# Kernel optimization log

Measured on AMD Instinct MI355X. Metric: run time of the kernel, lower is better.

Reference implementation:

```python
import jax, jax.numpy as jnp
import numpy as np

B, S, D = 4, 2048, 1024
H, DK, DV = 16, 64, 64
LN_EPS = 1e-5


def setup_inputs() -> dict:
    key = jax.random.key(0)
    ks = jax.random.split(key, 6)
    x = jax.random.normal(ks[0], (B, S, D), dtype=jnp.float32)
    # causal mask: True = masked position (j > i), broadcast over batch
    causal = jnp.triu(jnp.ones((S, S), dtype=bool), k=1)
    attention_mask = jnp.broadcast_to(causal, (B, S, S))
    scale = 1.0 / np.sqrt(D)
    w_q = jax.random.normal(ks[1], (D, H * DK), dtype=jnp.float32) * scale
    w_k = jax.random.normal(ks[2], (D, H * DK), dtype=jnp.float32) * scale
    w_v = jax.random.normal(ks[3], (D, H * DV), dtype=jnp.float32) * scale
    w_fc = jax.random.normal(ks[4], (H * DV, D), dtype=jnp.float32) * (1.0 / np.sqrt(H * DV))
    ln_gamma = jnp.ones((D,), dtype=jnp.float32)
    ln_beta = jnp.zeros((D,), dtype=jnp.float32)
    return {"x": x, "attention_mask": attention_mask, "w_q": w_q, "w_k": w_k,
            "w_v": w_v, "w_fc": w_fc, "ln_gamma": ln_gamma, "ln_beta": ln_beta}


def _layernorm(y, gamma, beta):
    mu = jnp.mean(y, axis=-1, keepdims=True)
    var = jnp.mean(jnp.square(y - mu), axis=-1, keepdims=True)
    return (y - mu) * jax.lax.rsqrt(var + LN_EPS) * gamma + beta


def reference(x, attention_mask, w_q, w_k, w_v, w_fc, ln_gamma, ln_beta):
    b, s, _ = x.shape
    # projections -> [b, h, s, dk/dv]
    q = (x @ w_q).reshape(b, s, H, DK).transpose(0, 2, 1, 3)
    k = (x @ w_k).reshape(b, s, H, DK).transpose(0, 2, 1, 3)
    v = (x @ w_v).reshape(b, s, H, DV).transpose(0, 2, 1, 3)
    # scaled dot-product attention with mask (True -> -1e9)
    scores = jnp.einsum('bhqd,bhkd->bhqk', q, k) / np.sqrt(DK)
    scores = jnp.where(attention_mask[:, None, :, :], jnp.float32(-1e9), scores)
    attn = jax.nn.softmax(scores, axis=-1)
    context = jnp.einsum('bhqk,bhkd->bhqd', attn, v)
    context = context.transpose(0, 2, 1, 3).reshape(b, s, H * DV)
    output = context @ w_fc
    out = _layernorm(output + x, ln_gamma, ln_beta)
    return out, attn
```

## Files before the change

kernel.cpp:

```cpp
#include <hip/hip_runtime.h>
#include <stdint.h>

#define S_LEN 2048
#define NHEAD 16

typedef short short8 __attribute__((ext_vector_type(8)));
typedef float f32x4 __attribute__((ext_vector_type(4)));
typedef unsigned short u16;

typedef __attribute__((address_space(1))) uint32_t AS1u32;
typedef __attribute__((address_space(3))) uint32_t AS3u32;

#define MFMA16(a, b, c) __builtin_amdgcn_mfma_f32_16x16x32_bf16((a), (b), (c), 0, 0, 0)

__device__ __forceinline__ void gload16(const void* g, void* l) {
  __builtin_amdgcn_global_load_lds((AS1u32*)g, (AS3u32*)l, 16, 0, 0);
}

__device__ __forceinline__ u16 f2bf(float f) {
  union { float f; uint32_t u; } c; c.f = f;
  return (u16)((c.u + 0x7fffu + ((c.u >> 16) & 1u)) >> 16);
}
__device__ __forceinline__ float bf2f(u16 h) {
  union { uint32_t u; float f; } c; c.u = ((uint32_t)h) << 16;
  return c.f;
}

__global__ __launch_bounds__(256) void conv_x_kernel(const float* __restrict__ x,
                                                     u16* __restrict__ xb) {
  size_t i = ((size_t)blockIdx.x * 256 + threadIdx.x) * 4;
  f32x4 v = *(const f32x4*)(x + i);
  union { u16 h[4]; uint2 d; } o;
  o.h[0] = f2bf(v[0]); o.h[1] = f2bf(v[1]); o.h[2] = f2bf(v[2]); o.h[3] = f2bf(v[3]);
  *(uint2*)(xb + i) = o.d;
}

__global__ __launch_bounds__(256) void transpose_w_kernel(
    const float* __restrict__ w0, const float* __restrict__ w1,
    const float* __restrict__ w2, const float* __restrict__ w3,
    u16* __restrict__ o0, u16* __restrict__ o1, u16* __restrict__ o2, u16* __restrict__ o3) {
  int z = blockIdx.z;
  const float* w = (z == 0) ? w0 : (z == 1) ? w1 : (z == 2) ? w2 : w3;
  u16* o = (z == 0) ? o0 : (z == 1) ? o1 : (z == 2) ? o2 : o3;
  float scale = (z == 0) ? 0.125f : 1.0f;
  __shared__ float t[32][33];
  int n0 = blockIdx.x * 32, k0 = blockIdx.y * 32;
  int tx = threadIdx.x & 31, ty = threadIdx.x >> 5;
#pragma unroll
  for (int i = 0; i < 4; ++i) {
    int k = ty * 4 + i;
    t[k][tx] = w[(size_t)(k0 + k) * 1024 + n0 + tx];
  }
  __syncthreads();
#pragma unroll
  for (int i = 0; i < 4; ++i) {
    int n = ty * 4 + i;
    o[(size_t)(n0 + n) * 1024 + k0 + tx] = f2bf(t[tx][n] * scale);
  }
}

__device__ __forceinline__ void gemm_stage(const char* Ab, const char* Bb, u16* As, u16* Bs,
                                           int m0, int n0, int kbyte, int tid) {
#pragma unroll
  for (int i = 0; i < 2; ++i) {
    int cid = i * 256 + tid;
    int row = cid >> 2, c = cid & 3;
    int off = kbyte + ((c ^ ((row >> 1) & 3)) << 4);
    gload16(Ab + (size_t)(m0 + row) * 2048 + off, (char*)As + i * 4096 + (tid & ~63) * 16);
    gload16(Bb + (size_t)(n0 + row) * 2048 + off, (char*)Bs + i * 4096 + (tid & ~63) * 16);
  }
}

__global__ __launch_bounds__(256) void gemm_bt_kernel(
    const u16* __restrict__ A, const u16* __restrict__ BT,
    void* __restrict__ out, int mode) {
  __shared__ u16 As[128 * 32];
  __shared__ u16 Bs[128 * 32];
  const int tid = threadIdx.x;
  const int lane = tid & 63, wv = tid >> 6;
  const int l15 = lane & 15, h16 = lane >> 4;
  const int wr = wv >> 1, wc = wv & 1;
  const int m0 = blockIdx.x * 128, n0 = blockIdx.y * 128;
  const char* Ab = (const char*)A;
  const char* Bb = (const char*)BT;

  f32x4 acc[4][4];
#pragma unroll
  for (int i = 0; i < 4; ++i)
#pragma unroll
    for (int j = 0; j < 4; ++j) acc[i][j] = (f32x4){0.f, 0.f, 0.f, 0.f};

  gemm_stage(Ab, Bb, As, Bs, m0, n0, 0, tid);
  for (int kt = 0; kt < 32; ++kt) {
    __syncthreads();
    short8 a[4], b[4];
#pragma unroll
    for (int mf = 0; mf < 4; ++mf) {
      int row = wr * 64 + mf * 16 + l15;
      a[mf] = *(const short8*)((const char*)As + row * 64 + ((h16 ^ ((row >> 1) & 3)) << 4));
    }
#pragma unroll
    for (int nf = 0; nf < 4; ++nf) {
      int row = wc * 64 + nf * 16 + l15;
      b[nf] = *(const short8*)((const char*)Bs + row * 64 + ((h16 ^ ((row >> 1) & 3)) << 4));
    }
#pragma unroll
    for (int mf = 0; mf < 4; ++mf)
#pragma unroll
      for (int nf = 0; nf < 4; ++nf)
        acc[mf][nf] = MFMA16(a[mf], b[nf], acc[mf][nf]);
    __syncthreads();
    if (kt + 1 < 32) gemm_stage(Ab, Bb, As, Bs, m0, n0, (kt + 1) * 64, tid);
  }

  if (mode == 0) {
    u16* o = (u16*)out;
#pragma unroll
    for (int mf = 0; mf < 4; ++mf)
#pragma unroll
      for (int nf = 0; nf < 4; ++nf)
#pragma unroll
        for (int r = 0; r < 4; ++r) {
          int m = m0 + wr * 64 + mf * 16 + 4 * h16 + r;
          int n = n0 + wc * 64 + nf * 16 + l15;
          int bb = m >> 11, s = m & 2047, hh = n >> 6, dk = n & 63;
          o[(((size_t)(bb * NHEAD + hh) * S_LEN + s) << 6) + dk] = f2bf(acc[mf][nf][r]);
        }
  } else {
    float* o = (float*)out;
#pragma unroll
    for (int mf = 0; mf < 4; ++mf)
#pragma unroll
      for (int nf = 0; nf < 4; ++nf)
#pragma unroll
        for (int r = 0; r < 4; ++r) {
          int m = m0 + wr * 64 + mf * 16 + 4 * h16 + r;
          int n = n0 + wc * 64 + nf * 16 + l15;
          o[(size_t)m * 1024 + n] = acc[mf][nf][r];
        }
  }
}

__global__ __launch_bounds__(256) void transpose_v_kernel(
    const u16* __restrict__ v, u16* __restrict__ vT) {
  __shared__ u16 t[64][80];
  int bh = blockIdx.y, s0 = blockIdx.x * 64;
  int tid = threadIdx.x;
  int sl = tid >> 2, c = tid & 3;
  const u16* src = v + (size_t)bh * S_LEN * 64 + (size_t)(s0 + sl) * 64 + c * 16;
  short8 a = *(const short8*)src;
  short8 b = *(const short8*)(src + 8);
#pragma unroll
  for (int j = 0; j < 8; ++j) {
    t[c * 16 + j][sl] = (u16)a[j];
    t[c * 16 + 8 + j][sl] = (u16)b[j];
  }
  __syncthreads();
  int dv = tid >> 2, c2 = tid & 3;
  u16* dst = vT + (size_t)bh * 64 * S_LEN + (size_t)dv * S_LEN + s0 + c2 * 16;
  *(short8*)dst = *(const short8*)&t[dv][c2 * 16];
  *(short8*)(dst + 8) = *(const short8*)&t[dv][c2 * 16 + 8];
}

__global__ __launch_bounds__(512) void attn_kernel(
    const u16* __restrict__ Q, const u16* __restrict__ K, const u16* __restrict__ VT,
    float* __restrict__ attn, u16* __restrict__ ctx) {
  __shared__ u16 Ks[128 * 64];
  __shared__ u16 QVs[128 * 64];
  __shared__ u16 Ps[128 * 128];

  const int tid = threadIdx.x;
  const int lane = tid & 63, wv = tid >> 6;
  const int l15 = lane & 15, h16 = lane >> 4;
  const int w16 = wv * 16;
  const int qt = blockIdx.x, bh = blockIdx.y;
  const int q0 = qt * 128;

  const char* Qb = (const char*)(Q + (size_t)bh * S_LEN * 64);
  const char* Kb = (const char*)(K + (size_t)bh * S_LEN * 64);
  const char* Vb = (const char*)(VT + (size_t)bh * 64 * S_LEN);
  float* attb = attn + (size_t)bh * S_LEN * S_LEN;

#pragma unroll
  for (int i = 0; i < 2; ++i) {
    int cid = i * 512 + tid;
    int row = cid >> 3, c = cid & 7;
    gload16(Qb + (size_t)(q0 + row) * 128 + ((c ^ (row & 7)) << 4),
            (char*)QVs + i * 8192 + (tid & ~63) * 16);
  }
  __syncthreads();
  short8 qf[2];
  {
    int row = w16 + l15;
    qf[0] = *(const short8*)((const char*)QVs + row * 128 + ((h16 ^ (row & 7)) << 4));
    qf[1] = *(const short8*)((const char*)QVs + row * 128 + (((4 + h16) ^ (row & 7)) << 4));
  }
  __syncthreads();

  float lsum[4] = {0.f, 0.f, 0.f, 0.f};
  for (int kvt = 0; kvt <= qt; ++kvt) {
    const int kv0 = kvt * 128;
#pragma unroll
    for (int i = 0; i < 2; ++i) {
      int cid = i * 512 + tid;
      int row = cid >> 3, c = cid & 7;
      gload16(Kb + (size_t)(kv0 + row) * 128 + ((c ^ (row & 7)) << 4),
              (char*)Ks + i * 8192 + (tid & ~63) * 16);
    }
    __syncthreads();
    f32x4 sc[8];
#pragma unroll
    for (int nf = 0; nf < 8; ++nf) sc[nf] = (f32x4){0.f, 0.f, 0.f, 0.f};
#pragma unroll
    for (int ks = 0; ks < 2; ++ks)
#pragma unroll
      for (int nf = 0; nf < 8; ++nf) {
        int row = nf * 16 + l15;
        short8 kb = *(const short8*)((const char*)Ks + row * 128 + (((ks * 4 + h16) ^ (row & 7)) << 4));
        sc[nf] = MFMA16(qf[ks], kb, sc[nf]);
      }
    if (kvt == qt) {
#pragma unroll
      for (int nf = 0; nf < 8; ++nf)
#pragma unroll
        for (int r = 0; r < 4; ++r)
          if (nf * 16 + l15 > w16 + 4 * h16 + r) sc[nf][r] = -1e30f;
    }
#pragma unroll
    for (int nf = 0; nf < 8; ++nf)
#pragma unroll
      for (int r = 0; r < 4; ++r) lsum[r] += __expf(sc[nf][r]);
    __syncthreads();
  }
#pragma unroll
  for (int r = 0; r < 4; ++r) {
    float v = lsum[r];
    v += __shfl_xor(v, 1);
    v += __shfl_xor(v, 2);
    v += __shfl_xor(v, 4);
    v += __shfl_xor(v, 8);
    lsum[r] = 1.0f / v;
  }

  f32x4 cacc[4];
#pragma unroll
  for (int nf = 0; nf < 4; ++nf) cacc[nf] = (f32x4){0.f, 0.f, 0.f, 0.f};

  for (int kvt = 0; kvt <= qt; ++kvt) {
    const int kv0 = kvt * 128;
#pragma unroll
    for (int i = 0; i < 2; ++i) {
      int cid = i * 512 + tid;
      int rowk = cid >> 3, ck = cid & 7;
      gload16(Kb + (size_t)(kv0 + rowk) * 128 + ((ck ^ (rowk & 7)) << 4),
              (char*)Ks + i * 8192 + (tid & ~63) * 16);
      int rowv = cid >> 4, cv = cid & 15;
      gload16(Vb + (size_t)rowv * 4096 + (size_t)kv0 * 2 + ((cv ^ (rowv & 7)) << 4),
              (char*)QVs + i * 8192 + (tid & ~63) * 16);
    }
    __syncthreads();
    f32x4 sc[8];
#pragma unroll
    for (int nf = 0; nf < 8; ++nf) sc[nf] = (f32x4){0.f, 0.f, 0.f, 0.f};
#pragma unroll
    for (int ks = 0; ks < 2; ++ks)
#pragma unroll
      for (int nf = 0; nf < 8; ++nf) {
        int row = nf * 16 + l15;
        short8 kb = *(const short8*)((const char*)Ks + row * 128 + (((ks * 4 + h16) ^ (row & 7)) << 4));
        sc[nf] = MFMA16(qf[ks], kb, sc[nf]);
      }
    if (kvt == qt) {
#pragma unroll
      for (int nf = 0; nf < 8; ++nf)
#pragma unroll
        for (int r = 0; r < 4; ++r)
          if (nf * 16 + l15 > w16 + 4 * h16 + r) sc[nf][r] = -1e30f;
    }
#pragma unroll
    for (int nf = 0; nf < 8; ++nf)
#pragma unroll
      for (int r = 0; r < 4; ++r) {
        float p = __expf(sc[nf][r]) * lsum[r];
        int rowL = w16 + 4 * h16 + r;
        int chunk = 2 * nf + (l15 >> 3);
        *(u16*)((char*)Ps + rowL * 256 + ((chunk ^ (rowL & 7)) << 4) + (l15 & 7) * 2) = f2bf(p);
      }
    __syncthreads();
#pragma unroll
    for (int ks = 0; ks < 4; ++ks) {
      int rowP = w16 + l15;
      short8 pa = *(const short8*)((const char*)Ps + rowP * 256 + (((ks * 4 + h16) ^ (rowP & 7)) << 4));
#pragma unroll
      for (int nf = 0; nf < 4; ++nf) {
        int rowV = nf * 16 + l15;
        short8 vb = *(const short8*)((const char*)QVs + rowV * 256 + (((ks * 4 + h16) ^ (rowV & 7)) << 4));
        cacc[nf] = MFMA16(pa, vb, cacc[nf]);
      }
    }
    {
      int row = tid >> 2, sub = tid & 3;
      const char* prow = (const char*)Ps + row * 256;
      float* arow = attb + (size_t)(q0 + row) * S_LEN + kv0;
#pragma unroll
      for (int c8 = 0; c8 < 4; ++c8) {
        int chunk = sub + 4 * c8;
        short8 pv = *(const short8*)(prow + ((chunk ^ (row & 7)) << 4));
        f32x4 f0 = {bf2f((u16)pv[0]), bf2f((u16)pv[1]), bf2f((u16)pv[2]), bf2f((u16)pv[3])};
        f32x4 f1 = {bf2f((u16)pv[4]), bf2f((u16)pv[5]), bf2f((u16)pv[6]), bf2f((u16)pv[7])};
        *(f32x4*)(arow + chunk * 8) = f0;
        *(f32x4*)(arow + chunk * 8 + 4) = f1;
      }
    }
    __syncthreads();
  }

  for (int kvt = qt + 1; kvt < 16; ++kvt) {
    const int kv0 = kvt * 128;
    int row = tid >> 2, sub = tid & 3;
    float* arow = attb + (size_t)(q0 + row) * S_LEN + kv0;
    f32x4 z = {0.f, 0.f, 0.f, 0.f};
#pragma unroll
    for (int c8 = 0; c8 < 4; ++c8) {
      int chunk = sub + 4 * c8;
      *(f32x4*)(arow + chunk * 8) = z;
      *(f32x4*)(arow + chunk * 8 + 4) = z;
    }
  }

  {
    int b = bh >> 4, hh = bh & 15;
#pragma unroll
    for (int nf = 0; nf < 4; ++nf)
#pragma unroll
      for (int r = 0; r < 4; ++r) {
        int qrow = q0 + w16 + 4 * h16 + r;
        ctx[((size_t)b * S_LEN + qrow) * 1024 + hh * 64 + nf * 16 + l15] = f2bf(cacc[nf][r]);
      }
  }
}

__global__ __launch_bounds__(256) void ln_kernel(float* __restrict__ io,
                                                 const float* __restrict__ x,
                                                 const float* __restrict__ gamma,
                                                 const float* __restrict__ beta) {
  int row = blockIdx.x, tid = threadIdx.x;
  size_t base = (size_t)row * 1024 + tid * 4;
  f32x4 p = *(const f32x4*)(io + base);
  f32x4 xv = *(const f32x4*)(x + base);
  f32x4 y;
  float s1 = 0.f, s2 = 0.f;
#pragma unroll
  for (int j = 0; j < 4; ++j) {
    y[j] = p[j] + xv[j];
    s1 += y[j];
    s2 += y[j] * y[j];
  }
#pragma unroll
  for (int off = 1; off <= 32; off <<= 1) {
    s1 += __shfl_xor(s1, off);
    s2 += __shfl_xor(s2, off);
  }
  __shared__ float r1[4], r2[4];
  int w = tid >> 6;
  if ((tid & 63) == 0) { r1[w] = s1; r2[w] = s2; }
  __syncthreads();
  float S1 = r1[0] + r1[1] + r1[2] + r1[3];
  float S2 = r2[0] + r2[1] + r2[2] + r2[3];
  float mu = S1 * (1.f / 1024.f);
  float var = S2 * (1.f / 1024.f) - mu * mu;
  float rs = rsqrtf(var + 1e-5f);
  f32x4 g = *(const f32x4*)(gamma + tid * 4);
  f32x4 bt = *(const f32x4*)(beta + tid * 4);
  f32x4 o;
#pragma unroll
  for (int j = 0; j < 4; ++j) o[j] = (y[j] - mu) * rs * g[j] + bt[j];
  *(f32x4*)(io + base) = o;
}

extern "C" void kernel_launch(void* const* d_in, const int* in_sizes, int n_in,
                              void* d_out, int out_size, void* d_ws, size_t ws_size,
                              hipStream_t stream) {
  (void)in_sizes; (void)n_in; (void)out_size; (void)ws_size;
  const float* x = (const float*)d_in[0];
  const float* wq = (const float*)d_in[2];
  const float* wk = (const float*)d_in[3];
  const float* wv = (const float*)d_in[4];
  const float* wfc = (const float*)d_in[5];
  const float* gamma = (const float*)d_in[6];
  const float* beta = (const float*)d_in[7];

  char* ws = (char*)d_ws;
  u16* xb = (u16*)ws;
  u16* wqT = (u16*)(ws + (16u << 20));
  u16* wkT = (u16*)(ws + (18u << 20));
  u16* wvT = (u16*)(ws + (20u << 20));
  u16* wfcT = (u16*)(ws + (22u << 20));
  u16* qb = (u16*)(ws + (24u << 20));
  u16* kb = (u16*)(ws + (40u << 20));
  u16* vb = (u16*)(ws + (56u << 20));
  u16* vT = (u16*)(ws + (72u << 20));
  u16* ctx = xb;

  float* outp = (float*)d_out;
  float* attnp = outp + (size_t)4 * 2048 * 1024;

  conv_x_kernel<<<8192, 256, 0, stream>>>(x, xb);
  transpose_w_kernel<<<dim3(32, 32, 4), 256, 0, stream>>>(wq, wk, wv, wfc, wqT, wkT, wvT, wfcT);
  gemm_bt_kernel<<<dim3(64, 8), 256, 0, stream>>>(xb, wqT, qb, 0);
  gemm_bt_kernel<<<dim3(64, 8), 256, 0, stream>>>(xb, wkT, kb, 0);
  gemm_bt_kernel<<<dim3(64, 8), 256, 0, stream>>>(xb, wvT, vb, 0);
  transpose_v_kernel<<<dim3(32, 64), 256, 0, stream>>>(vb, vT);
  attn_kernel<<<dim3(16, 64), 512, 0, stream>>>(qb, kb, vT, attnp, ctx);
  gemm_bt_kernel<<<dim3(64, 8), 256, 0, stream>>>(ctx, wfcT, outp, 1);
  ln_kernel<<<8192, 256, 0, stream>>>(outp, x, gamma, beta);
}
```

Measured before the change: 507.9 us.

## Fuse QKV GEMMs, split attention into denom and emit kernels, double-buffer K

Concatenates the Q/K/V weight transposes so one GEMM launch with a wider grid produces all three projections. Splits the attention kernel into a denominator pass that writes reciprocal row sums to workspace and an emit pass that reads them. Both passes double-buffer K tiles so the next tile loads while the current one is computed. The emit pass writes the large fp32 attention matrix with nontemporal stores to reduce cache pollution. The cost is an extra launch and a small global round trip for the row sums.

Result: slower. 721.4 us (+42.0%).

```diff
diff --git a/kernel.cpp b/kernel.cpp
--- a/kernel.cpp
+++ b/kernel.cpp
@@ -24,6 +24,10 @@
 __device__ __forceinline__ float bf2f(u16 h) {
   union { uint32_t u; float f; } c; c.u = ((uint32_t)h) << 16;
   return c.f;
+}
+
+__device__ __forceinline__ void nt_store4(float* p, f32x4 v) {
+  __builtin_nontemporal_store(v, (f32x4*)p);
 }
 
 __global__ __launch_bounds__(256) void conv_x_kernel(const float* __restrict__ x,
@@ -38,10 +42,10 @@
 __global__ __launch_bounds__(256) void transpose_w_kernel(
     const float* __restrict__ w0, const float* __restrict__ w1,
     const float* __restrict__ w2, const float* __restrict__ w3,
-    u16* __restrict__ o0, u16* __restrict__ o1, u16* __restrict__ o2, u16* __restrict__ o3) {
+    u16* __restrict__ qkvT, u16* __restrict__ fcT) {
   int z = blockIdx.z;
   const float* w = (z == 0) ? w0 : (z == 1) ? w1 : (z == 2) ? w2 : w3;
-  u16* o = (z == 0) ? o0 : (z == 1) ? o1 : (z == 2) ? o2 : o3;
+  u16* o = (z == 3) ? fcT : qkvT + (size_t)z * 1048576;
   float scale = (z == 0) ? 0.125f : 1.0f;
   __shared__ float t[32][33];
   int n0 = blockIdx.x * 32, k0 = blockIdx.y * 32;
@@ -123,8 +127,10 @@
         for (int r = 0; r < 4; ++r) {
           int m = m0 + wr * 64 + mf * 16 + 4 * h16 + r;
           int n = n0 + wc * 64 + nf * 16 + l15;
-          int bb = m >> 11, s = m & 2047, hh = n >> 6, dk = n & 63;
-          o[(((size_t)(bb * NHEAD + hh) * S_LEN + s) << 6) + dk] = f2bf(acc[mf][nf][r]);
+          int z = n >> 10, nn = n & 1023;
+          int bb = m >> 11, s = m & 2047, hh = nn >> 6, dk = nn & 63;
+          o[(size_t)z * 8388608 + (((size_t)(bb * NHEAD + hh) * S_LEN + s) << 6) + dk] =
+              f2bf(acc[mf][nf][r]);
         }
   } else {
     float* o = (float*)out;
@@ -162,52 +168,54 @@
   *(short8*)(dst + 8) = *(const short8*)&t[dv][c2 * 16 + 8];
 }
 
-__global__ __launch_bounds__(512) void attn_kernel(
-    const u16* __restrict__ Q, const u16* __restrict__ K, const u16* __restrict__ VT,
-    float* __restrict__ attn, u16* __restrict__ ctx) {
-  __shared__ u16 Ks[128 * 64];
-  __shared__ u16 QVs[128 * 64];
-  __shared__ u16 Ps[128 * 128];
-
+__device__ __forceinline__ void stage_qk(const char* base, int row0, u16* dst, int tid) {
+#pragma unroll
+  for (int i = 0; i < 2; ++i) {
+    int cid = i * 512 + tid;
+    int row = cid >> 3, c = cid & 7;
+    gload16(base + (size_t)(row0 + row) * 128 + ((c ^ (row & 7)) << 4),
+            (char*)dst + i * 8192 + (tid & ~63) * 16);
+  }
+}
+__device__ __forceinline__ void stage_v(const char* Vb, int kv0, u16* dst, int tid) {
+#pragma unroll
+  for (int i = 0; i < 2; ++i) {
+    int cid = i * 512 + tid;
+    int row = cid >> 4, c = cid & 15;
+    gload16(Vb + (size_t)row * 4096 + (size_t)kv0 * 2 + ((c ^ (row & 7)) << 4),
+            (char*)dst + i * 8192 + (tid & ~63) * 16);
+  }
+}
+
+__global__ __launch_bounds__(512) void denom_kernel(
+    const u16* __restrict__ Q, const u16* __restrict__ K, float* __restrict__ rinv) {
+  __shared__ u16 Qs[128 * 64];
+  __shared__ u16 Ks[2][128 * 64];
   const int tid = threadIdx.x;
   const int lane = tid & 63, wv = tid >> 6;
   const int l15 = lane & 15, h16 = lane >> 4;
   const int w16 = wv * 16;
   const int qt = blockIdx.x, bh = blockIdx.y;
   const int q0 = qt * 128;
-
   const char* Qb = (const char*)(Q + (size_t)bh * S_LEN * 64);
   const char* Kb = (const char*)(K + (size_t)bh * S_LEN * 64);
-  const char* Vb = (const char*)(VT + (size_t)bh * 64 * S_LEN);
-  float* attb = attn + (size_t)bh * S_LEN * S_LEN;
-
-#pragma unroll
-  for (int i = 0; i < 2; ++i) {
-    int cid = i * 512 + tid;
-    int row = cid >> 3, c = cid & 7;
-    gload16(Qb + (size_t)(q0 + row) * 128 + ((c ^ (row & 7)) << 4),
-            (char*)QVs + i * 8192 + (tid & ~63) * 16);
-  }
+
+  stage_qk(Qb, q0, Qs, tid);
+  stage_qk(Kb, 0, Ks[0], tid);
   __syncthreads();
   short8 qf[2];
   {
     int row = w16 + l15;
-    qf[0] = *(const short8*)((const char*)QVs + row * 128 + ((h16 ^ (row & 7)) << 4));
-    qf[1] = *(const short8*)((const char*)QVs + row * 128 + (((4 + h16) ^ (row & 7)) << 4));
+    qf[0] = *(const short8*)((const char*)Qs + row * 128 + ((h16 ^ (row & 7)) << 4));
+    qf[1] = *(const short8*)((const char*)Qs + row * 128 + (((4 + h16) ^ (row & 7)) << 4));
   }
   __syncthreads();
 
   float lsum[4] = {0.f, 0.f, 0.f, 0.f};
-  for (int kvt = 0; kvt <= qt; ++kvt) {
-    const int kv0 = kvt * 128;
-#pragma unroll
-    for (int i = 0; i < 2; ++i) {
-      int cid = i * 512 + tid;
-      int row = cid >> 3, c = cid & 7;
-      gload16(Kb + (size_t)(kv0 + row) * 128 + ((c ^ (row & 7)) << 4),
-              (char*)Ks + i * 8192 + (tid & ~63) * 16);
-    }
-    __syncthreads();
+  int cur = 0;
+  for (int t = 0; t <= qt; ++t) {
+    if (t + 1 <= qt) stage_qk(Kb, (t + 1) * 128, Ks[cur ^ 1], tid);
+    const char* Kc = (const char*)Ks[cur];
     f32x4 sc[8];
 #pragma unroll
     for (int nf = 0; nf < 8; ++nf) sc[nf] = (f32x4){0.f, 0.f, 0.f, 0.f};
@@ -216,10 +224,10 @@
 #pragma unroll
       for (int nf = 0; nf < 8; ++nf) {
         int row = nf * 16 + l15;
-        short8 kb = *(const short8*)((const char*)Ks + row * 128 + (((ks * 4 + h16) ^ (row & 7)) << 4));
+        short8 kb = *(const short8*)(Kc + row * 128 + (((ks * 4 + h16) ^ (row & 7)) << 4));
         sc[nf] = MFMA16(qf[ks], kb, sc[nf]);
       }
-    if (kvt == qt) {
+    if (t == qt) {
 #pragma unroll
       for (int nf = 0; nf < 8; ++nf)
 #pragma unroll
@@ -231,6 +239,7 @@
 #pragma unroll
       for (int r = 0; r < 4; ++r) lsum[r] += __expf(sc[nf][r]);
     __syncthreads();
+    cur ^= 1;
   }
 #pragma unroll
   for (int r = 0; r < 4; ++r) {
@@ -239,26 +248,54 @@
     v += __shfl_xor(v, 2);
     v += __shfl_xor(v, 4);
     v += __shfl_xor(v, 8);
-    lsum[r] = 1.0f / v;
-  }
+    lsum[r] = v;
+  }
+  if (l15 == 0) {
+    f32x4 o = {1.f / lsum[0], 1.f / lsum[1], 1.f / lsum[2], 1.f / lsum[3]};
+    *(f32x4*)(rinv + (size_t)bh * S_LEN + q0 + w16 + 4 * h16) = o;
+  }
+}
+
+__global__ __launch_bounds__(512) void emit_kernel(
+    const u16* __restrict__ Q, const u16* __restrict__ K, const u16* __restrict__ VT,
+    const float* __restrict__ rinv, float* __restrict__ attn, u16* __restrict__ ctx) {
+  __shared__ u16 Ks[2][128 * 64];
+  __shared__ u16 Vs[64 * 128];
+  __shared__ u16 Ps[128 * 128];
+
+  const int tid = threadIdx.x;
+  const int lane = tid & 63, wv = tid >> 6;
+  const int l15 = lane & 15, h16 = lane >> 4;
+  const int w16 = wv * 16;
+  const int qt = blockIdx.x, bh = blockIdx.y;
+  const int q0 = qt * 128;
+
+  const char* Qb = (const char*)(Q + (size_t)bh * S_LEN * 64);
+  const char* Kb = (const char*)(K + (size_t)bh * S_LEN * 64);
+  const char* Vb = (const char*)(VT + (size_t)bh * 64 * S_LEN);
+  float* attb = attn + (size_t)bh * S_LEN * S_LEN;
+
+  stage_qk(Qb, q0, Ps, tid);
+  stage_qk(Kb, 0, Ks[0], tid);
+  __syncthreads();
+  short8 qf[2];
+  {
+    int row = w16 + l15;
+    qf[0] = *(const short8*)((const char*)Ps + row * 128 + ((h16 ^ (row & 7)) << 4));
+    qf[1] = *(const short8*)((const char*)Ps + row * 128 + (((4 + h16) ^ (row & 7)) << 4));
+  }
+  f32x4 ri = *(const f32x4*)(rinv + (size_t)bh * S_LEN + q0 + w16 + 4 * h16);
+  __syncthreads();
 
   f32x4 cacc[4];
 #pragma unroll
   for (int nf = 0; nf < 4; ++nf) cacc[nf] = (f32x4){0.f, 0.f, 0.f, 0.f};
 
-  for (int kvt = 0; kvt <= qt; ++kvt) {
-    const int kv0 = kvt * 128;
-#pragma unroll
-    for (int i = 0; i < 2; ++i) {
-      int cid = i * 512 + tid;
-      int rowk = cid >> 3, ck = cid & 7;
-      gload16(Kb + (size_t)(kv0 + rowk) * 128 + ((ck ^ (rowk & 7)) << 4),
-              (char*)Ks + i * 8192 + (tid & ~63) * 16);
-      int rowv = cid >> 4, cv = cid & 15;
-      gload16(Vb + (size_t)rowv * 4096 + (size_t)kv0 * 2 + ((cv ^ (rowv & 7)) << 4),
-              (char*)QVs + i * 8192 + (tid & ~63) * 16);
-    }
-    __syncthreads();
+  int cur = 0;
+  for (int t = 0; t <= qt; ++t) {
+    const int kv0 = t * 128;
+    stage_v(Vb, kv0, Vs, tid);
+    const char* Kc = (const char*)Ks[cur];
     f32x4 sc[8];
 #pragma unroll
     for (int nf = 0; nf < 8; ++nf) sc[nf] = (f32x4){0.f, 0.f, 0.f, 0.f};
@@ -267,10 +304,10 @@
 #pragma unroll
       for (int nf = 0; nf < 8; ++nf) {
         int row = nf * 16 + l15;
-        short8 kb = *(const short8*)((const char*)Ks + row * 128 + (((ks * 4 + h16) ^ (row & 7)) << 4));
+        short8 kb = *(const short8*)(Kc + row * 128 + (((ks * 4 + h16) ^ (row & 7)) << 4));
         sc[nf] = MFMA16(qf[ks], kb, sc[nf]);
       }
-    if (kvt == qt) {
+    if (t == qt) {
 #pragma unroll
       for (int nf = 0; nf < 8; ++nf)
 #pragma unroll
@@ -281,12 +318,13 @@
     for (int nf = 0; nf < 8; ++nf)
 #pragma unroll
       for (int r = 0; r < 4; ++r) {
-        float p = __expf(sc[nf][r]) * lsum[r];
+        float p = __expf(sc[nf][r]) * ri[r];
         int rowL = w16 + 4 * h16 + r;
         int chunk = 2 * nf + (l15 >> 3);
         *(u16*)((char*)Ps + rowL * 256 + ((chunk ^ (rowL & 7)) << 4) + (l15 & 7) * 2) = f2bf(p);
       }
     __syncthreads();
+    if (t + 1 <= qt) stage_qk(Kb, kv0 + 128, Ks[cur ^ 1], tid);
 #pragma unroll
     for (int ks = 0; ks < 4; ++ks) {
       int rowP = w16 + l15;
@@ -294,8 +332,8 @@
 #pragma unroll
       for (int nf = 0; nf < 4; ++nf) {
         int rowV = nf * 16 + l15;
-        short8 vb = *(const short8*)((const char*)QVs + rowV * 256 + (((ks * 4 + h16) ^ (rowV & 7)) << 4));
-        cacc[nf] = MFMA16(pa, vb, cacc[nf]);
+        short8 vbf = *(const short8*)((const char*)Vs + rowV * 256 + (((ks * 4 + h16) ^ (rowV & 7)) << 4));
+        cacc[nf] = MFMA16(pa, vbf, cacc[nf]);
       }
     }
     {
@@ -308,11 +346,12 @@
         short8 pv = *(const short8*)(prow + ((chunk ^ (row & 7)) << 4));
         f32x4 f0 = {bf2f((u16)pv[0]), bf2f((u16)pv[1]), bf2f((u16)pv[2]), bf2f((u16)pv[3])};
         f32x4 f1 = {bf2f((u16)pv[4]), bf2f((u16)pv[5]), bf2f((u16)pv[6]), bf2f((u16)pv[7])};
-        *(f32x4*)(arow + chunk * 8) = f0;
-        *(f32x4*)(arow + chunk * 8 + 4) = f1;
+        nt_store4(arow + chunk * 8, f0);
+        nt_store4(arow + chunk * 8 + 4, f1);
       }
     }
     __syncthreads();
+    cur ^= 1;
   }
 
   for (int kvt = qt + 1; kvt < 16; ++kvt) {
@@ -323,8 +362,8 @@
 #pragma unroll
     for (int c8 = 0; c8 < 4; ++c8) {
       int chunk = sub + 4 * c8;
-      *(f32x4*)(arow + chunk * 8) = z;
-      *(f32x4*)(arow + chunk * 8 + 4) = z;
+      nt_store4(arow + chunk * 8, z);
+      nt_store4(arow + chunk * 8 + 4, z);
     }
   }
 
@@ -392,26 +431,25 @@
 
   char* ws = (char*)d_ws;
   u16* xb = (u16*)ws;
-  u16* wqT = (u16*)(ws + (16u << 20));
-  u16* wkT = (u16*)(ws + (18u << 20));
-  u16* wvT = (u16*)(ws + (20u << 20));
+  u16* wqkvT = (u16*)(ws + (16u << 20));
   u16* wfcT = (u16*)(ws + (22u << 20));
-  u16* qb = (u16*)(ws + (24u << 20));
-  u16* kb = (u16*)(ws + (40u << 20));
-  u16* vb = (u16*)(ws + (56u << 20));
+  u16* qkvb = (u16*)(ws + (24u << 20));
+  u16* qb = qkvb;
+  u16* kb = qkvb + (size_t)8388608;
+  u16* vb = qkvb + (size_t)16777216;
   u16* vT = (u16*)(ws + (72u << 20));
+  float* rinvp = (float*)(ws + (56u << 20));
   u16* ctx = xb;
 
   float* outp = (float*)d_out;
   float* attnp = outp + (size_t)4 * 2048 * 1024;
 
   conv_x_kernel<<<8192, 256, 0, stream>>>(x, xb);
-  transpose_w_kernel<<<dim3(32, 32, 4), 256, 0, stream>>>(wq, wk, wv, wfc, wqT, wkT, wvT, wfcT);
-  gemm_bt_kernel<<<dim3(64, 8), 256, 0, stream>>>(xb, wqT, qb, 0);
-  gemm_bt_kernel<<<dim3(64, 8), 256, 0, stream>>>(xb, wkT, kb, 0);
-  gemm_bt_kernel<<<dim3(64, 8), 256, 0, stream>>>(xb, wvT, vb, 0);
+  transpose_w_kernel<<<dim3(32, 32, 4), 256, 0, stream>>>(wq, wk, wv, wfc, wqkvT, wfcT);
+  gemm_bt_kernel<<<dim3(64, 24), 256, 0, stream>>>(xb, wqkvT, qkvb, 0);
   transpose_v_kernel<<<dim3(32, 64), 256, 0, stream>>>(vb, vT);
-  attn_kernel<<<dim3(16, 64), 512, 0, stream>>>(qb, kb, vT, attnp, ctx);
+  denom_kernel<<<dim3(16, 64), 512, 0, stream>>>(qb, kb, rinvp);
+  emit_kernel<<<dim3(16, 64), 512, 0, stream>>>(qb, kb, vT, rinvp, attnp, ctx);
   gemm_bt_kernel<<<dim3(64, 8), 256, 0, stream>>>(ctx, wfcT, outp, 1);
   ln_kernel<<<8192, 256, 0, stream>>>(outp, x, gamma, beta);
 }
```
